# Kernel optimization log

Hardware: AMD Instinct MI355X
Metric: run time of the kernel (lower is better)

## Reference

```python
import jax, jax.numpy as jnp
import numpy as np

B, T, C, H = 8, 4096, 384, 64

def setup_inputs() -> dict:
    key = jax.random.key(0)
    k1, k2, k3, k4 = jax.random.split(key, 4)
    x = jax.random.normal(k1, (B, T, C), dtype=jnp.float32)
    # nn.Linear(C, H, bias=False) weight applied as x @ W (W stored [C, H])
    s = 1.0 / np.sqrt(C)
    Wk = jax.random.normal(k2, (C, H), dtype=jnp.float32) * s
    Wq = jax.random.normal(k3, (C, H), dtype=jnp.float32) * s
    Wv = jax.random.normal(k4, (C, H), dtype=jnp.float32) * s
    return {"x": x, "Wk": Wk, "Wq": Wq, "Wv": Wv}

def reference(x, Wk, Wq, Wv):
    Bx, Tx, Cx = x.shape
    k = x @ Wk  # [B,T,H]
    q = x @ Wq  # [B,T,H]
    v = x @ Wv  # [B,T,H]
    # NOTE: original scales by C**-0.5 (embedding dim), not head_size**-0.5
    w = jnp.einsum('bth,bsh->bts', q, k) * (Cx ** -0.5)  # [B,T,T]
    causal = jnp.tril(jnp.ones((Tx, Tx), dtype=bool))
    w = jnp.where(causal, w, -jnp.inf)
    w = jax.nn.softmax(w, axis=-1)
    # dropout omitted (eval mode / deterministic reference)
    out = jnp.einsum('bts,bsh->bth', w, v)  # [B,T,H]
    return out
```

## Files before the change

### kernel.cpp

```cpp
#include <hip/hip_runtime.h>
#include <hip/hip_bf16.h>


typedef __bf16 bf16x8 __attribute__((ext_vector_type(8)));
typedef float  f32x4  __attribute__((ext_vector_type(4)));

#define BB   8
#define TT   4096
#define CC   384
#define HH   64
#define NROW (BB*TT)
#define QSCALE (0.05103103630798288f * 1.4426950408889634f)

#if __has_builtin(__builtin_amdgcn_exp2f)
#define EXP2(x) __builtin_amdgcn_exp2f(x)
#else
#define EXP2(x) exp2f(x)
#endif

__device__ __forceinline__ unsigned short f2bf(float f) {
    __bf16 h = (__bf16)f;
    return __builtin_bit_cast(unsigned short, h);
}

__global__ __launch_bounds__(256) void wtrans_kernel(
        const float* __restrict__ Wk,
        const float* __restrict__ Wq,
        const float* __restrict__ Wv,
        unsigned short* __restrict__ Wt) {
    __shared__ __align__(16) unsigned short tile[64][72];
    const float* Wm = (blockIdx.y == 0) ? Wk : ((blockIdx.y == 1) ? Wq : Wv);
    unsigned short* Wtm = Wt + blockIdx.y * (HH * CC);
    const int c0 = blockIdx.x * 64;
#pragma unroll
    for (int i = 0; i < 16; ++i) {
        int id = threadIdx.x + i * 256;
        int c = id >> 6, h = id & 63;
        tile[c][h] = f2bf(Wm[(c0 + c) * HH + h]);
    }
    __syncthreads();
#pragma unroll
    for (int i = 0; i < 16; ++i) {
        int id = threadIdx.x + i * 256;
        int h = id >> 6, c = id & 63;
        Wtm[h * CC + c0 + c] = tile[c][h];
    }
}

__global__ __launch_bounds__(256, 1) void qkv_kernel(
        const float* __restrict__ x,
        const unsigned short* __restrict__ Wt,
        unsigned short* __restrict__ q_ws,
        unsigned short* __restrict__ k_ws,
        unsigned short* __restrict__ vt_ws) {
    __shared__ __align__(16) float xs[6][32][64];
    __shared__ __align__(16) unsigned short vtile[64][40];

    const int lane = threadIdx.x & 63;
    const int wv   = threadIdx.x >> 6;
    const int rt   = wv & 1;
    const int hh   = wv >> 1;
    const int l15  = lane & 15;
    const int quad = lane >> 4;
    const int rb   = blockIdx.x * 32;
    const int ntb  = hh * 2;

#pragma unroll
    for (int kk = 0; kk < 6; ++kk) {
#pragma unroll
        for (int j = 0; j < 2; ++j) {
            const int r0 = wv * 8 + j * 4;
            const int r  = r0 + quad;
            const int ch = l15 ^ (r & 7);
            const float* src = x + (long)(rb + r) * CC + kk * 64 + ch * 4;
            float* dst = &xs[kk][r0][0];
            __builtin_amdgcn_global_load_lds(
                (const __attribute__((address_space(1))) unsigned int*)src,
                (__attribute__((address_space(3))) unsigned int*)dst,
                16, 0, 0);
        }
    }

    bf16x8 bf[2][12];
    auto loadW = [&](int kk, bf16x8* dst) {
#pragma unroll
        for (int m = 0; m < 3; ++m)
#pragma unroll
            for (int n = 0; n < 2; ++n)
#pragma unroll
                for (int h01 = 0; h01 < 2; ++h01)
                    dst[m * 4 + n * 2 + h01] = *reinterpret_cast<const bf16x8*>(
                        Wt + m * (HH * CC) + ((ntb + n) * 16 + l15) * CC
                          + kk * 64 + h01 * 32 + quad * 8);
    };
    loadW(0, bf[0]);

    f32x4 acc[3][2];
    const f32x4 zero = {0.f, 0.f, 0.f, 0.f};
#pragma unroll
    for (int m = 0; m < 3; ++m)
#pragma unroll
        for (int n = 0; n < 2; ++n) acc[m][n] = zero;

    const int rloc = rt * 16 + l15;
    const int rx7  = rloc & 7;

    __asm volatile("s_waitcnt vmcnt(0)" ::: "memory");
    __syncthreads();

#pragma unroll
    for (int kk = 0; kk < 6; ++kk) {
        if (kk < 5) {
            loadW(kk + 1, bf[(kk + 1) & 1]);
            __asm volatile("" ::: "memory");
        }
#pragma unroll
        for (int h01 = 0; h01 < 2; ++h01) {
            const int chb = 8 * h01 + 2 * quad;
            const f32x4 xa = *reinterpret_cast<const f32x4*>(
                &xs[kk][rloc][((chb) ^ rx7) * 4]);
            const f32x4 xb = *reinterpret_cast<const f32x4*>(
                &xs[kk][rloc][((chb + 1) ^ rx7) * 4]);
            bf16x8 a;
#pragma unroll
            for (int e = 0; e < 4; ++e) {
                a[e]     = (__bf16)xa[e];
                a[4 + e] = (__bf16)xb[e];
            }
#pragma unroll
            for (int m = 0; m < 3; ++m)
#pragma unroll
                for (int n = 0; n < 2; ++n)
                    acc[m][n] = __builtin_amdgcn_mfma_f32_16x16x32_bf16(
                        a, bf[kk & 1][m * 4 + n * 2 + h01], acc[m][n], 0, 0, 0);
        }
    }

#pragma unroll
    for (int n = 0; n < 2; ++n) {
        const int nt = ntb + n;
        const int h  = nt * 16 + l15;
        const int c8 = h >> 3;
        const int jj = h & 7;
#pragma unroll
        for (int r = 0; r < 4; ++r) {
            const int gr = rb + rt * 16 + quad * 4 + r;
            const int s   = gr & 63;
            const int stp = ((s >> 4) & 2) + ((s >> 2) & 1);
            const int ip  = ((s >> 1) & 12) + (s & 3);
            k_ws[(long)(gr >> 6) * 4096 + stp * 1024 + c8 * 128 + ip * 8 + jj]
                = f2bf(acc[0][n][r]);
            q_ws[gr * HH + h] = f2bf(acc[1][n][r] * QSCALE);
            vtile[h][rt * 16 + quad * 4 + r] = f2bf(acc[2][n][r]);
        }
    }
    __syncthreads();
    {
        const int id  = threadIdx.x;
        const int dt  = id >> 6, scl = (id >> 4) & 3, ii = id & 15;
        const int sc  = scl + ((rb >> 3) & 4);
        unsigned short* dst = vt_ws + (long)(rb >> 6) * 4096
                              + (dt * 8 + sc) * 128 + ii * 8;
        *reinterpret_cast<uint4*>(dst) =
            *reinterpret_cast<const uint4*>(&vtile[dt * 16 + ii][scl * 8]);
    }
}

__global__ __launch_bounds__(512, 4) void attn_kernel(
        const unsigned short* __restrict__ q_ws,
        const unsigned short* __restrict__ k_ws,
        const unsigned short* __restrict__ vt_ws,
        float* __restrict__ out) {
    __shared__ __align__(16) float xchg[64 * 65];
    __shared__ float mx1[64], lx1[64];

    const int lane = threadIdx.x & 63;
    const int wv8  = threadIdx.x >> 6;
    const int grp  = wv8 >> 2;
    const int wg   = wv8 & 3;
    const int l15  = lane & 15;
    const int quad = lane >> 4;

    const int bid = blockIdx.x;
    const int b   = bid & 7;
    const int qt  = 63 - (bid >> 3);

    const f32x4 zero = {0.f, 0.f, 0.f, 0.f};

    auto do_tile = [&](int t, int qrow,
                       const bf16x8& qf0, const bf16x8& qf1,
                       f32x4* o, float& mprev, float& lsum) {
        const int s0 = t * 64;
        const unsigned short* ktile = k_ws + ((long)((b * TT + s0) >> 4)) * 1024;
        const unsigned short* vtile = vt_ws + ((long)((b * TT + s0) >> 6)) * 4096;

        bf16x8 ka0[4], ka1[4];
#pragma unroll
        for (int st = 0; st < 4; ++st) {
            ka0[st] = *reinterpret_cast<const bf16x8*>(
                ktile + ((st * 8 + quad) * 16 + l15) * 8);
            ka1[st] = *reinterpret_cast<const bf16x8*>(
                ktile + ((st * 8 + 4 + quad) * 16 + l15) * 8);
        }
        bf16x8 vb0[4], vb1[4];
#pragma unroll
        for (int dt = 0; dt < 4; ++dt) {
            vb0[dt] = *reinterpret_cast<const bf16x8*>(
                vtile + dt * 1024 + quad * 128 + l15 * 8);
            vb1[dt] = *reinterpret_cast<const bf16x8*>(
                vtile + dt * 1024 + (4 + quad) * 128 + l15 * 8);
        }

        f32x4 sc[4];
        __builtin_amdgcn_s_setprio(1);
#pragma unroll
        for (int st = 0; st < 4; ++st) {
            f32x4 z = zero;
            z = __builtin_amdgcn_mfma_f32_16x16x32_bf16(ka0[st], qf0, z, 0, 0, 0);
            z = __builtin_amdgcn_mfma_f32_16x16x32_bf16(ka1[st], qf1, z, 0, 0, 0);
            sc[st] = z;
        }
        __builtin_amdgcn_s_setprio(0);

        if (t == qt) {
#pragma unroll
            for (int st = 0; st < 4; ++st)
#pragma unroll
                for (int r = 0; r < 4; ++r) {
                    int sg = s0 + ((st >> 1) << 5) + (quad << 3)
                               + ((st & 1) << 2) + r;
                    if (sg > qrow) sc[st][r] = -1e30f;
                }
        }

        float mloc = -1e30f;
#pragma unroll
        for (int st = 0; st < 4; ++st)
#pragma unroll
            for (int r = 0; r < 4; ++r) mloc = fmaxf(mloc, sc[st][r]);
        mloc = fmaxf(mloc, __shfl_xor(mloc, 16));
        mloc = fmaxf(mloc, __shfl_xor(mloc, 32));

        if (!__all(mloc <= mprev + 8.0f)) {
            const float mnew = fmaxf(mprev, mloc);
            const float alpha = EXP2(mprev - mnew);
            lsum *= alpha;
            float ar[4];
#pragma unroll
            for (int r = 0; r < 4; ++r) ar[r] = __shfl(alpha, quad * 4 + r);
#pragma unroll
            for (int dt = 0; dt < 4; ++dt)
#pragma unroll
                for (int r = 0; r < 4; ++r) o[dt][r] *= ar[r];
            mprev = mnew;
        }

        float psum = 0.f;
#pragma unroll
        for (int st = 0; st < 4; ++st)
#pragma unroll
            for (int r = 0; r < 4; ++r) {
                float pv = EXP2(sc[st][r] - mprev);
                psum += pv;
                sc[st][r] = pv;
            }
        lsum += psum;

        bf16x8 pf0, pf1;
#pragma unroll
        for (int r = 0; r < 4; ++r) {
            pf0[r]     = (__bf16)sc[0][r];
            pf0[4 + r] = (__bf16)sc[1][r];
            pf1[r]     = (__bf16)sc[2][r];
            pf1[4 + r] = (__bf16)sc[3][r];
        }
        __builtin_amdgcn_s_setprio(1);
#pragma unroll
        for (int dt = 0; dt < 4; ++dt) {
            o[dt] = __builtin_amdgcn_mfma_f32_16x16x32_bf16(pf0, vb0[dt], o[dt], 0, 0, 0);
            o[dt] = __builtin_amdgcn_mfma_f32_16x16x32_bf16(pf1, vb1[dt], o[dt], 0, 0, 0);
        }
        __builtin_amdgcn_s_setprio(0);
    };

    {
        const int qrow = qt * 64 + wg * 16 + l15;
        const unsigned short* qbase = q_ws + (b * TT + qrow) * HH;
        const bf16x8 qf0 = *reinterpret_cast<const bf16x8*>(qbase + quad * 8);
        const bf16x8 qf1 = *reinterpret_cast<const bf16x8*>(qbase + 32 + quad * 8);
        f32x4 o[4];
#pragma unroll
        for (int dt = 0; dt < 4; ++dt) o[dt] = zero;
        float mprev = -1e30f, lsum = 0.f;
        for (int t = grp; t <= qt; t += 2)
            do_tile(t, qrow, qf0, qf1, o, mprev, lsum);

        lsum += __shfl_xor(lsum, 16);
        lsum += __shfl_xor(lsum, 32);

        __syncthreads();
        if (grp == 1) {
            if (quad == 0) { mx1[wg * 16 + l15] = mprev; lx1[wg * 16 + l15] = lsum; }
#pragma unroll
            for (int dt = 0; dt < 4; ++dt)
#pragma unroll
                for (int r = 0; r < 4; ++r)
                    xchg[(wg * 16 + quad * 4 + r) * 65 + dt * 16 + l15] = o[dt][r];
        }
        __syncthreads();
        if (grp == 0) {
#pragma unroll
            for (int r = 0; r < 4; ++r) {
                const int row = wg * 16 + quad * 4 + r;
                const float m0r = __shfl(mprev, quad * 4 + r);
                const float m1r = mx1[row];
                const float ms  = fmaxf(m0r, m1r);
                const float w0  = EXP2(m0r - ms);
                const float w1  = EXP2(m1r - ms);
#pragma unroll
                for (int dt = 0; dt < 4; ++dt)
                    o[dt][r] = o[dt][r] * w0 + xchg[row * 65 + dt * 16 + l15] * w1;
            }
            const float m1l = mx1[wg * 16 + l15];
            const float msl = fmaxf(mprev, m1l);
            lsum = EXP2(mprev - msl) * lsum + EXP2(m1l - msl) * lx1[wg * 16 + l15];

            float rl[4];
#pragma unroll
            for (int r = 0; r < 4; ++r) rl[r] = 1.0f / __shfl(lsum, quad * 4 + r);
            const int orow = qt * 64 + wg * 16 + quad * 4;
#pragma unroll
            for (int dt = 0; dt < 4; ++dt)
#pragma unroll
                for (int r = 0; r < 4; ++r)
                    out[(long)(b * TT + orow + r) * HH + dt * 16 + l15] = o[dt][r] * rl[r];
        }
    }
}

extern "C" void kernel_launch(void* const* d_in, const int* in_sizes, int n_in,
                              void* d_out, int out_size, void* d_ws, size_t ws_size,
                              hipStream_t stream) {
    const float* x  = (const float*)d_in[0];
    const float* Wk = (const float*)d_in[1];
    const float* Wq = (const float*)d_in[2];
    const float* Wv = (const float*)d_in[3];
    float* out = (float*)d_out;

    char* ws = (char*)d_ws;
    unsigned short* Wt    = (unsigned short*)(ws);
    unsigned short* q_ws  = (unsigned short*)(ws + 147456);
    unsigned short* k_ws  = (unsigned short*)(ws + 147456 + 4194304);
    unsigned short* vt_ws = (unsigned short*)(ws + 147456 + 2 * 4194304);

    wtrans_kernel<<<dim3(6, 3), 256, 0, stream>>>(Wk, Wq, Wv, Wt);
    qkv_kernel<<<NROW / 32, 256, 0, stream>>>(x, Wt, q_ws, k_ws, vt_ws);
    attn_kernel<<<(TT / 64) * BB, 512, 0, stream>>>(q_ws, k_ws, vt_ws, out);
}
```

Before: 170.3 us.

## Pair causal query tiles per block and split KV over eight wave groups

```diff
diff --git a/kernel.cpp b/kernel.cpp
--- a/kernel.cpp
+++ b/kernel.cpp
@@ -166,30 +166,84 @@
     }
 }
 
-__global__ __launch_bounds__(512, 4) void attn_kernel(
+__global__ __launch_bounds__(1024, 4) void attn_kernel(
         const unsigned short* __restrict__ q_ws,
         const unsigned short* __restrict__ k_ws,
         const unsigned short* __restrict__ vt_ws,
         float* __restrict__ out) {
-    __shared__ __align__(16) float xchg[64 * 65];
-    __shared__ float mx1[64], lx1[64];
+    __shared__ __align__(16) float xbuf[4][64][65];
+    __shared__ float mxb[4][64], lxb[4][64];
 
     const int lane = threadIdx.x & 63;
-    const int wv8  = threadIdx.x >> 6;
-    const int grp  = wv8 >> 2;
-    const int wg   = wv8 & 3;
+    const int wv16 = threadIdx.x >> 6;
+    const int g    = wv16 >> 1;
+    const int rh   = wv16 & 1;
     const int l15  = lane & 15;
     const int quad = lane >> 4;
 
     const int bid = blockIdx.x;
     const int b   = bid & 7;
-    const int qt  = 63 - (bid >> 3);
+    const int p   = bid >> 3;
 
     const f32x4 zero = {0.f, 0.f, 0.f, 0.f};
 
-    auto do_tile = [&](int t, int qrow,
-                       const bf16x8& qf0, const bf16x8& qf1,
-                       f32x4* o, float& mprev, float& lsum) {
+    auto sm_pv = [&](f32x4* sc, f32x4* o, float& m, float& l,
+                     const bf16x8* vb0, const bf16x8* vb1) {
+        float mloc = -1e30f;
+#pragma unroll
+        for (int st = 0; st < 4; ++st)
+#pragma unroll
+            for (int r = 0; r < 4; ++r) mloc = fmaxf(mloc, sc[st][r]);
+        mloc = fmaxf(mloc, __shfl_xor(mloc, 16));
+        mloc = fmaxf(mloc, __shfl_xor(mloc, 32));
+
+        if (!__all(mloc <= m + 8.0f)) {
+            const float mnew = fmaxf(m, mloc);
+            const float alpha = EXP2(m - mnew);
+            l *= alpha;
+            float ar[4];
+#pragma unroll
+            for (int r = 0; r < 4; ++r) ar[r] = __shfl(alpha, quad * 4 + r);
+#pragma unroll
+            for (int dt = 0; dt < 4; ++dt)
+#pragma unroll
+                for (int r = 0; r < 4; ++r) o[dt][r] *= ar[r];
+            m = mnew;
+        }
+
+        float psum = 0.f;
+#pragma unroll
+        for (int st = 0; st < 4; ++st)
+#pragma unroll
+            for (int r = 0; r < 4; ++r) {
+                float pv = EXP2(sc[st][r] - m);
+                psum += pv;
+                sc[st][r] = pv;
+            }
+        l += psum;
+
+        bf16x8 pf0, pf1;
+#pragma unroll
+        for (int r = 0; r < 4; ++r) {
+            pf0[r]     = (__bf16)sc[0][r];
+            pf0[4 + r] = (__bf16)sc[1][r];
+            pf1[r]     = (__bf16)sc[2][r];
+            pf1[4 + r] = (__bf16)sc[3][r];
+        }
+        __builtin_amdgcn_s_setprio(1);
+#pragma unroll
+        for (int dt = 0; dt < 4; ++dt) {
+            o[dt] = __builtin_amdgcn_mfma_f32_16x16x32_bf16(pf0, vb0[dt], o[dt], 0, 0, 0);
+            o[dt] = __builtin_amdgcn_mfma_f32_16x16x32_bf16(pf1, vb1[dt], o[dt], 0, 0, 0);
+        }
+        __builtin_amdgcn_s_setprio(0);
+    };
+
+    auto do_tile = [&](int t, int qt, int qrowA,
+                       const bf16x8& qfA0, const bf16x8& qfA1,
+                       const bf16x8& qfB0, const bf16x8& qfB1,
+                       f32x4* oA, f32x4* oB,
+                       float& mA, float& lA, float& mB, float& lB) {
         const int s0 = t * 64;
         const unsigned short* ktile = k_ws + ((long)((b * TT + s0) >> 4)) * 1024;
         const unsigned short* vtile = vt_ws + ((long)((b * TT + s0) >> 6)) * 4096;
@@ -202,6 +256,26 @@
             ka1[st] = *reinterpret_cast<const bf16x8*>(
                 ktile + ((st * 8 + 4 + quad) * 16 + l15) * 8);
         }
+
+        f32x4 scA[4], scB[4];
+        __builtin_amdgcn_s_setprio(1);
+#pragma unroll
+        for (int st = 0; st < 4; ++st) {
+            f32x4 z = zero;
+            z = __builtin_amdgcn_mfma_f32_16x16x32_bf16(ka0[st], qfA0, z, 0, 0, 0);
+            z = __builtin_amdgcn_mfma_f32_16x16x32_bf16(ka1[st], qfA1, z, 0, 0, 0);
+            scA[st] = z;
+        }
+#pragma unroll
+        for (int st = 0; st < 4; ++st) {
+            f32x4 z = zero;
+            z = __builtin_amdgcn_mfma_f32_16x16x32_bf16(ka0[st], qfB0, z, 0, 0, 0);
+            z = __builtin_amdgcn_mfma_f32_16x16x32_bf16(ka1[st], qfB1, z, 0, 0, 0);
+            scB[st] = z;
+        }
+        __builtin_amdgcn_s_setprio(0);
+        __asm volatile("" ::: "memory");
+
         bf16x8 vb0[4], vb1[4];
 #pragma unroll
         for (int dt = 0; dt < 4; ++dt) {
@@ -211,17 +285,6 @@
                 vtile + dt * 1024 + (4 + quad) * 128 + l15 * 8);
         }
 
-        f32x4 sc[4];
-        __builtin_amdgcn_s_setprio(1);
-#pragma unroll
-        for (int st = 0; st < 4; ++st) {
-            f32x4 z = zero;
-            z = __builtin_amdgcn_mfma_f32_16x16x32_bf16(ka0[st], qf0, z, 0, 0, 0);
-            z = __builtin_amdgcn_mfma_f32_16x16x32_bf16(ka1[st], qf1, z, 0, 0, 0);
-            sc[st] = z;
-        }
-        __builtin_amdgcn_s_setprio(0);
-
         if (t == qt) {
 #pragma unroll
             for (int st = 0; st < 4; ++st)
@@ -229,113 +292,119 @@
                 for (int r = 0; r < 4; ++r) {
                     int sg = s0 + ((st >> 1) << 5) + (quad << 3)
                                + ((st & 1) << 2) + r;
-                    if (sg > qrow) sc[st][r] = -1e30f;
-                }
-        }
-
-        float mloc = -1e30f;
-#pragma unroll
-        for (int st = 0; st < 4; ++st)
-#pragma unroll
-            for (int r = 0; r < 4; ++r) mloc = fmaxf(mloc, sc[st][r]);
-        mloc = fmaxf(mloc, __shfl_xor(mloc, 16));
-        mloc = fmaxf(mloc, __shfl_xor(mloc, 32));
-
-        if (!__all(mloc <= mprev + 8.0f)) {
-            const float mnew = fmaxf(mprev, mloc);
-            const float alpha = EXP2(mprev - mnew);
-            lsum *= alpha;
-            float ar[4];
-#pragma unroll
-            for (int r = 0; r < 4; ++r) ar[r] = __shfl(alpha, quad * 4 + r);
+                    if (sg > qrowA)      scA[st][r] = -1e30f;
+                    if (sg > qrowA + 16) scB[st][r] = -1e30f;
+                }
+        }
+
+        sm_pv(scA, oA, mA, lA, vb0, vb1);
+        sm_pv(scB, oB, mB, lB, vb0, vb1);
+    };
+
+    auto run_phase = [&](int qt) {
+        const int qrowA = qt * 64 + rh * 32 + l15;
+        const unsigned short* qbA = q_ws + (b * TT + qrowA) * HH;
+        const unsigned short* qbB = qbA + 16 * HH;
+        const bf16x8 qfA0 = *reinterpret_cast<const bf16x8*>(qbA + quad * 8);
+        const bf16x8 qfA1 = *reinterpret_cast<const bf16x8*>(qbA + 32 + quad * 8);
+        const bf16x8 qfB0 = *reinterpret_cast<const bf16x8*>(qbB + quad * 8);
+        const bf16x8 qfB1 = *reinterpret_cast<const bf16x8*>(qbB + 32 + quad * 8);
+
+        f32x4 oA[4], oB[4];
+#pragma unroll
+        for (int dt = 0; dt < 4; ++dt) { oA[dt] = zero; oB[dt] = zero; }
+        float mA = -1e30f, lA = 0.f, mB = -1e30f, lB = 0.f;
+
+        for (int t = g; t <= qt; t += 8)
+            do_tile(t, qt, qrowA, qfA0, qfA1, qfB0, qfB1, oA, oB, mA, lA, mB, lB);
+
+        lA += __shfl_xor(lA, 16); lA += __shfl_xor(lA, 32);
+        lB += __shfl_xor(lB, 16); lB += __shfl_xor(lB, 32);
+
+#pragma unroll
+        for (int round = 0; round < 3; ++round) {
+            const int step = 1 << round;
+            const bool active = (g & (step - 1)) == 0;
+            const bool writer = active && (g & step);
+            const int bx = g >> (round + 1);
+            __syncthreads();
+            if (writer) {
+                if (quad == 0) {
+                    mxb[bx][rh * 32 + l15]      = mA; lxb[bx][rh * 32 + l15]      = lA;
+                    mxb[bx][rh * 32 + 16 + l15] = mB; lxb[bx][rh * 32 + 16 + l15] = lB;
+                }
+#pragma unroll
+                for (int dt = 0; dt < 4; ++dt)
+#pragma unroll
+                    for (int r = 0; r < 4; ++r) {
+                        xbuf[bx][rh * 32 + quad * 4 + r][dt * 16 + l15]      = oA[dt][r];
+                        xbuf[bx][rh * 32 + 16 + quad * 4 + r][dt * 16 + l15] = oB[dt][r];
+                    }
+            }
+            __syncthreads();
+            if (active && !writer) {
+#pragma unroll
+                for (int r = 0; r < 4; ++r) {
+                    const int row = rh * 32 + quad * 4 + r;
+                    const float m0r = __shfl(mA, quad * 4 + r);
+                    const float m1r = mxb[bx][row];
+                    const float ms  = fmaxf(m0r, m1r);
+                    const float w0  = EXP2(m0r - ms);
+                    const float w1  = EXP2(m1r - ms);
+#pragma unroll
+                    for (int dt = 0; dt < 4; ++dt)
+                        oA[dt][r] = oA[dt][r] * w0 + xbuf[bx][row][dt * 16 + l15] * w1;
+                }
+                {
+                    const float m1l = mxb[bx][rh * 32 + l15];
+                    const float msl = fmaxf(mA, m1l);
+                    lA = EXP2(mA - msl) * lA + EXP2(m1l - msl) * lxb[bx][rh * 32 + l15];
+                    mA = msl;
+                }
+#pragma unroll
+                for (int r = 0; r < 4; ++r) {
+                    const int row = rh * 32 + 16 + quad * 4 + r;
+                    const float m0r = __shfl(mB, quad * 4 + r);
+                    const float m1r = mxb[bx][row];
+                    const float ms  = fmaxf(m0r, m1r);
+                    const float w0  = EXP2(m0r - ms);
+                    const float w1  = EXP2(m1r - ms);
+#pragma unroll
+                    for (int dt = 0; dt < 4; ++dt)
+                        oB[dt][r] = oB[dt][r] * w0 + xbuf[bx][row][dt * 16 + l15] * w1;
+                }
+                {
+                    const float m1l = mxb[bx][rh * 32 + 16 + l15];
+                    const float msl = fmaxf(mB, m1l);
+                    lB = EXP2(mB - msl) * lB + EXP2(m1l - msl) * lxb[bx][rh * 32 + 16 + l15];
+                    mB = msl;
+                }
+            }
+        }
+
+        if (g == 0) {
+            float rlA[4], rlB[4];
+#pragma unroll
+            for (int r = 0; r < 4; ++r) {
+                rlA[r] = 1.0f / __shfl(lA, quad * 4 + r);
+                rlB[r] = 1.0f / __shfl(lB, quad * 4 + r);
+            }
+            const int orowA = qt * 64 + rh * 32 + quad * 4;
 #pragma unroll
             for (int dt = 0; dt < 4; ++dt)
 #pragma unroll
-                for (int r = 0; r < 4; ++r) o[dt][r] *= ar[r];
-            mprev = mnew;
-        }
-
-        float psum = 0.f;
-#pragma unroll
-        for (int st = 0; st < 4; ++st)
-#pragma unroll
-            for (int r = 0; r < 4; ++r) {
-                float pv = EXP2(sc[st][r] - mprev);
-                psum += pv;
-                sc[st][r] = pv;
-            }
-        lsum += psum;
-
-        bf16x8 pf0, pf1;
-#pragma unroll
-        for (int r = 0; r < 4; ++r) {
-            pf0[r]     = (__bf16)sc[0][r];
-            pf0[4 + r] = (__bf16)sc[1][r];
-            pf1[r]     = (__bf16)sc[2][r];
-            pf1[4 + r] = (__bf16)sc[3][r];
-        }
-        __builtin_amdgcn_s_setprio(1);
-#pragma unroll
-        for (int dt = 0; dt < 4; ++dt) {
-            o[dt] = __builtin_amdgcn_mfma_f32_16x16x32_bf16(pf0, vb0[dt], o[dt], 0, 0, 0);
-            o[dt] = __builtin_amdgcn_mfma_f32_16x16x32_bf16(pf1, vb1[dt], o[dt], 0, 0, 0);
-        }
-        __builtin_amdgcn_s_setprio(0);
+                for (int r = 0; r < 4; ++r) {
+                    out[(long)(b * TT + orowA + r) * HH + dt * 16 + l15]
+                        = oA[dt][r] * rlA[r];
+                    out[(long)(b * TT + orowA + 16 + r) * HH + dt * 16 + l15]
+                        = oB[dt][r] * rlB[r];
+                }
+        }
+        __syncthreads();
     };
 
-    {
-        const int qrow = qt * 64 + wg * 16 + l15;
-        const unsigned short* qbase = q_ws + (b * TT + qrow) * HH;
-        const bf16x8 qf0 = *reinterpret_cast<const bf16x8*>(qbase + quad * 8);
-        const bf16x8 qf1 = *reinterpret_cast<const bf16x8*>(qbase + 32 + quad * 8);
-        f32x4 o[4];
-#pragma unroll
-        for (int dt = 0; dt < 4; ++dt) o[dt] = zero;
-        float mprev = -1e30f, lsum = 0.f;
-        for (int t = grp; t <= qt; t += 2)
-            do_tile(t, qrow, qf0, qf1, o, mprev, lsum);
-
-        lsum += __shfl_xor(lsum, 16);
-        lsum += __shfl_xor(lsum, 32);
-
-        __syncthreads();
-        if (grp == 1) {
-            if (quad == 0) { mx1[wg * 16 + l15] = mprev; lx1[wg * 16 + l15] = lsum; }
-#pragma unroll
-            for (int dt = 0; dt < 4; ++dt)
-#pragma unroll
-                for (int r = 0; r < 4; ++r)
-                    xchg[(wg * 16 + quad * 4 + r) * 65 + dt * 16 + l15] = o[dt][r];
-        }
-        __syncthreads();
-        if (grp == 0) {
-#pragma unroll
-            for (int r = 0; r < 4; ++r) {
-                const int row = wg * 16 + quad * 4 + r;
-                const float m0r = __shfl(mprev, quad * 4 + r);
-                const float m1r = mx1[row];
-                const float ms  = fmaxf(m0r, m1r);
-                const float w0  = EXP2(m0r - ms);
-                const float w1  = EXP2(m1r - ms);
-#pragma unroll
-                for (int dt = 0; dt < 4; ++dt)
-                    o[dt][r] = o[dt][r] * w0 + xchg[row * 65 + dt * 16 + l15] * w1;
-            }
-            const float m1l = mx1[wg * 16 + l15];
-            const float msl = fmaxf(mprev, m1l);
-            lsum = EXP2(mprev - msl) * lsum + EXP2(m1l - msl) * lx1[wg * 16 + l15];
-
-            float rl[4];
-#pragma unroll
-            for (int r = 0; r < 4; ++r) rl[r] = 1.0f / __shfl(lsum, quad * 4 + r);
-            const int orow = qt * 64 + wg * 16 + quad * 4;
-#pragma unroll
-            for (int dt = 0; dt < 4; ++dt)
-#pragma unroll
-                for (int r = 0; r < 4; ++r)
-                    out[(long)(b * TT + orow + r) * HH + dt * 16 + l15] = o[dt][r] * rl[r];
-        }
-    }
+    run_phase(63 - p);
+    run_phase(p);
 }
 
 extern "C" void kernel_launch(void* const* d_in, const int* in_sizes, int n_in,
@@ -355,5 +424,5 @@
 
     wtrans_kernel<<<dim3(6, 3), 256, 0, stream>>>(Wk, Wq, Wv, Wt);
     qkv_kernel<<<NROW / 32, 256, 0, stream>>>(x, Wt, q_ws, k_ws, vt_ws);
-    attn_kernel<<<(TT / 64) * BB, 512, 0, stream>>>(q_ws, k_ws, vt_ws, out);
+    attn_kernel<<<(TT / 128) * BB, 1024, 0, stream>>>(q_ws, k_ws, vt_ws, out);
 }
```

New measurement: 230.0 us. +35.0%, slower.
